# Kernel tuning notes

Hardware: AMD Instinct MI355X
Metric: run time of the kernel (lower is better)

The kernel has to match this reference:

```python
import jax, jax.numpy as jnp
import numpy as np

B, S, D = 1, 2048, 1024   # batch, seq, hidden_size
I = 2048                  # intermediate_size (mlp1 emits 2*I, SwiGLU halves)
E = 8                     # num_experts
K = 2                     # experts_per_token
LIMIT = 7.0               # swiglu_limit
ALPHA = 1.702             # gpt-oss swiglu alpha
EPS = 1e-5                # RMSNorm eps


def setup_inputs() -> dict:
    key = jax.random.key(0)
    ks = jax.random.split(key, 4)
    s = 0.02
    return {
        "x": jax.random.normal(ks[0], (B, S, D), jnp.float32),
        "norm_scale": jnp.ones((D,), jnp.float32),
        "gate_w": jax.random.normal(ks[1], (D, E), jnp.float32) * s,
        "gate_b": jnp.zeros((E,), jnp.float32),
        "mlp1_w": jax.random.normal(ks[2], (E, D, 2 * I), jnp.float32) * s,
        "mlp1_b": jnp.zeros((E, 2 * I), jnp.float32),
        "mlp2_w": jax.random.normal(ks[3], (E, I, D), jnp.float32) * s,
        "mlp2_b": jnp.zeros((E, D), jnp.float32),
    }


def _swiglu(h):
    # gpt-oss interleaved SwiGLU with clamp limit
    x_glu = jnp.minimum(h[..., ::2], LIMIT)
    x_lin = jnp.clip(h[..., 1::2], -LIMIT, LIMIT)
    return x_glu * jax.nn.sigmoid(ALPHA * x_glu) * (x_lin + 1.0)


def _moe(t, gate_w, gate_b, mlp1_w, mlp1_b, mlp2_w, mlp2_b):
    T = t.shape[0]
    logits = t @ gate_w + gate_b                 # [T, E]
    top_v, top_i = jax.lax.top_k(logits, K)      # [T, K]
    probs = jax.nn.softmax(top_v, axis=-1)       # softmax over selected experts
    # dense routing-weight matrix, zero for unselected experts
    w = jnp.zeros((T, E), t.dtype).at[jnp.arange(T)[:, None], top_i].set(probs)

    def body(acc, ew):
        w1, b1, w2, b2, we = ew                  # per-expert params + weights [T]
        h = _swiglu(t @ w1 + b1)                 # [T, I]
        y = h @ w2 + b2                          # [T, D]
        return acc + we[:, None] * y, None

    acc0 = jnp.zeros((T, t.shape[1]), t.dtype)
    acc, _ = jax.lax.scan(body, acc0, (mlp1_w, mlp1_b, mlp2_w, mlp2_b, w.T))
    return acc


def reference(x, norm_scale, gate_w, gate_b, mlp1_w, mlp1_b, mlp2_w, mlp2_b):
    Bx, Sx, Dx = x.shape
    ms = jnp.mean(x * x, axis=-1, keepdims=True)
    t = (x * jax.lax.rsqrt(ms + EPS) * norm_scale).reshape(Bx * Sx, Dx)
    y = _moe(t, gate_w, gate_b, mlp1_w, mlp1_b, mlp2_w, mlp2_b)
    return x + y.reshape(Bx, Sx, Dx)
```

## Files before the change

### kernel.cpp

```cpp
#include <hip/hip_runtime.h>
#include <hip/hip_bf16.h>

typedef unsigned short u16;
typedef __attribute__((ext_vector_type(4))) unsigned short u16x4;
typedef __attribute__((ext_vector_type(8))) unsigned short u16x8;
typedef __attribute__((ext_vector_type(8))) short bf16x8;
typedef __attribute__((ext_vector_type(4))) float f32x4;

#define DEV static __device__ __forceinline__

DEV float bf2f(u16 b){ union{unsigned u; float f;} c; c.u = ((unsigned)b) << 16; return c.f; }
DEV u16 f2bf(float f){ union{float f; unsigned u;} c; c.f = f; unsigned u = c.u; u += 0x7FFF + ((u >> 16) & 1); return (u16)(u >> 16); }
DEV u16 f2bfh(float f){ union { __hip_bfloat16 h; u16 u; } c; c.h = __float2bfloat16(f); return c.u; }
DEV float getc(float4 v, int c){ return c == 0 ? v.x : c == 1 ? v.y : c == 2 ? v.z : v.w; }

DEV void gload16(const void* g, void* l){
  __builtin_amdgcn_global_load_lds((const __attribute__((address_space(1))) unsigned int*)g,
                                   (__attribute__((address_space(3))) unsigned int*)l, 16, 0, 0);
}

__global__ __launch_bounds__(256) void k_rms(
    const float* __restrict__ x, const float* __restrict__ nsc,
    const float* __restrict__ gw, const float* __restrict__ gb,
    u16* __restrict__ t, int* __restrict__ topi, float* __restrict__ topp)
{
  const int token = blockIdx.x, tid = threadIdx.x;
  const int wv = tid >> 6, lane = tid & 63;
  const float4 xv = *(const float4*)&x[(size_t)token * 1024 + tid * 4];
  float f[4] = {xv.x, xv.y, xv.z, xv.w};
  float ss = f[0]*f[0] + f[1]*f[1] + f[2]*f[2] + f[3]*f[3];
  #pragma unroll
  for (int o = 32; o > 0; o >>= 1) ss += __shfl_down(ss, o, 64);
  __shared__ float red[4];
  __shared__ float s_rs;
  if (lane == 0) red[wv] = ss;
  __syncthreads();
  if (tid == 0) s_rs = rsqrtf((red[0] + red[1] + red[2] + red[3]) * (1.0f / 1024.0f) + 1e-5f);
  __syncthreads();
  const float rs = s_rs;
  const float4 sv = *(const float4*)&nsc[tid * 4];
  const float sc[4] = {sv.x, sv.y, sv.z, sv.w};
  float tf[4]; u16x4 tv;
  #pragma unroll
  for (int j = 0; j < 4; ++j){ tf[j] = f[j] * rs * sc[j]; tv[j] = f2bf(tf[j]); }
  *(u16x4*)&t[(size_t)token * 1024 + tid * 4] = tv;

  float la[8] = {0,0,0,0,0,0,0,0};
  #pragma unroll
  for (int j = 0; j < 4; ++j){
    const int k = tid * 4 + j;
    const float4 g0 = *(const float4*)&gw[k * 8];
    const float4 g1 = *(const float4*)&gw[k * 8 + 4];
    la[0] += tf[j] * g0.x; la[1] += tf[j] * g0.y; la[2] += tf[j] * g0.z; la[3] += tf[j] * g0.w;
    la[4] += tf[j] * g1.x; la[5] += tf[j] * g1.y; la[6] += tf[j] * g1.z; la[7] += tf[j] * g1.w;
  }
  #pragma unroll
  for (int o = 32; o > 0; o >>= 1)
    #pragma unroll
    for (int e = 0; e < 8; ++e) la[e] += __shfl_down(la[e], o, 64);
  __shared__ float lred[4][8];
  if (lane == 0){
    #pragma unroll
    for (int e = 0; e < 8; ++e) lred[wv][e] = la[e];
  }
  __syncthreads();
  if (tid == 0){
    float lg[8];
    #pragma unroll
    for (int e = 0; e < 8; ++e) lg[e] = lred[0][e] + lred[1][e] + lred[2][e] + lred[3][e] + gb[e];
    int i0 = 0;
    for (int e = 1; e < 8; ++e) if (lg[e] > lg[i0]) i0 = e;
    int i1 = -1;
    for (int e = 0; e < 8; ++e) if (e != i0 && (i1 < 0 || lg[e] > lg[i1])) i1 = e;
    const float d = __expf(lg[i1] - lg[i0]);
    const float p0 = 1.0f / (1.0f + d);
    topi[token * 2] = i0; topi[token * 2 + 1] = i1;
    topp[token * 2] = p0; topp[token * 2 + 1] = d * p0;
  }
}

__global__ __launch_bounds__(256) void k_route(
    const int* __restrict__ topi, const float* __restrict__ topp,
    int* __restrict__ cnt, int* __restrict__ offs, int* __restrict__ tok_of,
    float* __restrict__ wt_of, int* __restrict__ slot_of, int* __restrict__ posg)
{
  __shared__ int c[8];
  __shared__ int o[8];
  const int tid = threadIdx.x;
  if (tid < 8) c[tid] = 0;
  __syncthreads();
  for (int a = tid; a < 4096; a += 256){
    int e = topi[a];
    posg[a] = atomicAdd(&c[e], 1);
  }
  __syncthreads();
  if (tid == 0){
    int run = 0;
    for (int e = 0; e < 8; ++e){ o[e] = run; offs[e] = run; cnt[e] = c[e]; run += c[e]; }
  }
  __syncthreads();
  for (int a = tid; a < 4096; a += 256){
    int e = topi[a];
    int s = o[e] + posg[a];
    tok_of[s] = a >> 1;
    wt_of[s] = topp[a];
    slot_of[a] = s;
  }
}

__global__ __launch_bounds__(256) void k_gemm1(
    const u16* __restrict__ t, const float* __restrict__ w1, const float* __restrict__ b1,
    const int* __restrict__ cnt, const int* __restrict__ offs, const int* __restrict__ tok_of,
    u16* __restrict__ h)
{
  const int e = blockIdx.z;
  const int count = cnt[e];
  const int m0 = blockIdx.y * 128;
  if (m0 >= count) return;
  const int off = offs[e];
  const int n0 = blockIdx.x * 128;

  __shared__ __attribute__((aligned(16))) u16 As[128 * 64];
  __shared__ __attribute__((aligned(16))) u16 Bs[128 * 64];

  const int tid = threadIdx.x, wv = tid >> 6, lane = tid & 63;
  const int arl = lane >> 3;
  const int axu = (lane & 7) ^ arl;

  const u16* asrc[4];
  u16* adst[4];
  #pragma unroll
  for (int i = 0; i < 4; ++i){
    const int rr = i * 32 + wv * 8 + arl;
    int r = m0 + rr; if (r > count - 1) r = count - 1;
    asrc[i] = t + (size_t)tok_of[off + r] * 1024 + axu * 8;
    adst[i] = &As[(i * 32 + wv * 8) * 64];
  }

  const int tkq = tid >> 5;
  const int tnb = (tid & 31) * 4;
  const float* bsrc = w1 + (size_t)e * (1024 * 4096) + (size_t)(tkq * 8) * 4096 + n0 + tnb;

  const int wm = wv & 1, wn = wv >> 1;
  const int fr = lane & 15, q = lane >> 4;

  f32x4 acc[4][4];
  #pragma unroll
  for (int a = 0; a < 4; ++a)
    #pragma unroll
    for (int b = 0; b < 4; ++b) acc[a][b] = (f32x4){0.f, 0.f, 0.f, 0.f};

  for (int k0 = 0; k0 < 1024; k0 += 64){
    #pragma unroll
    for (int i = 0; i < 4; ++i){ gload16(asrc[i], adst[i]); asrc[i] += 64; }
    const float4 fv0 = *(const float4*)(bsrc);
    const float4 fv1 = *(const float4*)(bsrc + 4096);
    const float4 fv2 = *(const float4*)(bsrc + 2 * 4096);
    const float4 fv3 = *(const float4*)(bsrc + 3 * 4096);
    const float4 fv4 = *(const float4*)(bsrc + 4 * 4096);
    const float4 fv5 = *(const float4*)(bsrc + 5 * 4096);
    const float4 fv6 = *(const float4*)(bsrc + 6 * 4096);
    const float4 fv7 = *(const float4*)(bsrc + 7 * 4096);
    bsrc += (size_t)64 * 4096;
    #pragma unroll
    for (int c = 0; c < 4; ++c){
      const int nr = tnb + c;
      u16x8 wq;
      wq[0] = f2bfh(getc(fv0, c)); wq[1] = f2bfh(getc(fv1, c));
      wq[2] = f2bfh(getc(fv2, c)); wq[3] = f2bfh(getc(fv3, c));
      wq[4] = f2bfh(getc(fv4, c)); wq[5] = f2bfh(getc(fv5, c));
      wq[6] = f2bfh(getc(fv6, c)); wq[7] = f2bfh(getc(fv7, c));
      *(u16x8*)((char*)Bs + nr * 128 + ((tkq ^ ((nr >> 1) & 7)) << 4)) = wq;
    }
    __syncthreads();
    #pragma unroll
    for (int hh = 0; hh < 2; ++hh){
      const int puA = (((hh * 4) + q) ^ (fr & 7)) * 8;
      const int puB = (((hh * 4) + q) ^ ((fr >> 1) & 7)) * 8;
      bf16x8 af[4], bq[4];
      #pragma unroll
      for (int fm = 0; fm < 4; ++fm) af[fm] = *(const bf16x8*)&As[(wm * 64 + fm * 16 + fr) * 64 + puA];
      #pragma unroll
      for (int fn = 0; fn < 4; ++fn) bq[fn] = *(const bf16x8*)&Bs[(wn * 64 + fn * 16 + fr) * 64 + puB];
      #pragma unroll
      for (int fm = 0; fm < 4; ++fm)
        #pragma unroll
        for (int fn = 0; fn < 4; ++fn)
          acc[fm][fn] = __builtin_amdgcn_mfma_f32_16x16x32_bf16(af[fm], bq[fn], acc[fm][fn], 0, 0, 0);
    }
    __syncthreads();
  }

  const int cb = n0 + wn * 64 + fr;
  float b1v[4];
  #pragma unroll
  for (int fn = 0; fn < 4; ++fn) b1v[fn] = b1[e * 4096 + cb + fn * 16];
  const int rq = q * 4;
  const bool ev = ((lane & 1) == 0);
  #pragma unroll
  for (int fm = 0; fm < 4; ++fm)
    #pragma unroll
    for (int fn = 0; fn < 4; ++fn)
      #pragma unroll
      for (int r = 0; r < 4; ++r){
        const float val = acc[fm][fn][r] + b1v[fn];
        const float oth = __shfl_xor(val, 1, 64);
        if (ev){
          const int row = m0 + wm * 64 + fm * 16 + rq + r;
          if (row < count){
            const float g = fminf(val, 7.0f);
            const float l = fminf(fmaxf(oth, -7.0f), 7.0f);
            const float o = g / (1.0f + __expf(-1.702f * g)) * (l + 1.0f);
            h[(size_t)(off + row) * 2048 + ((cb + fn * 16) >> 1)] = f2bf(o);
          }
        }
      }
}

__global__ __launch_bounds__(256) void k_gemm2(
    const u16* __restrict__ h, const float* __restrict__ w2, const float* __restrict__ b2,
    const int* __restrict__ cnt, const int* __restrict__ offs, const float* __restrict__ wt_of,
    u16* __restrict__ ys)
{
  const int e = blockIdx.z;
  const int count = cnt[e];
  const int m0 = blockIdx.y * 128;
  if (m0 >= count) return;
  const int off = offs[e];
  const int n0 = blockIdx.x * 64;

  __shared__ __attribute__((aligned(16))) u16 As[128 * 64];
  __shared__ __attribute__((aligned(16))) u16 Bs[64 * 64];

  const int tid = threadIdx.x, wv = tid >> 6, lane = tid & 63;
  const int arl = lane >> 3;
  const int axu = (lane & 7) ^ arl;

  const u16* asrc[4];
  u16* adst[4];
  #pragma unroll
  for (int i = 0; i < 4; ++i){
    const int rr = i * 32 + wv * 8 + arl;
    int r = m0 + rr; if (r > count - 1) r = count - 1;
    asrc[i] = h + (size_t)(off + r) * 2048 + axu * 8;
    adst[i] = &As[(i * 32 + wv * 8) * 64];
  }

  const int tkq = tid >> 4;
  const int tnb = (tid & 15) * 4;
  const float* bsrc = w2 + (size_t)e * (2048 * 1024) + (size_t)(tkq * 4) * 1024 + n0 + tnb;

  const int wm = wv & 1, wn = wv >> 1;
  const int fr = lane & 15, q = lane >> 4;

  f32x4 acc[4][2];
  #pragma unroll
  for (int a = 0; a < 4; ++a)
    #pragma unroll
    for (int b = 0; b < 2; ++b) acc[a][b] = (f32x4){0.f, 0.f, 0.f, 0.f};

  for (int k0 = 0; k0 < 2048; k0 += 64){
    #pragma unroll
    for (int i = 0; i < 4; ++i){ gload16(asrc[i], adst[i]); asrc[i] += 64; }
    const float4 g0 = *(const float4*)(bsrc);
    const float4 g1 = *(const float4*)(bsrc + 1024);
    const float4 g2 = *(const float4*)(bsrc + 2 * 1024);
    const float4 g3 = *(const float4*)(bsrc + 3 * 1024);
    bsrc += (size_t)64 * 1024;
    #pragma unroll
    for (int c = 0; c < 4; ++c){
      const int nr = tnb + c;
      u16x4 wd;
      wd[0] = f2bfh(getc(g0, c)); wd[1] = f2bfh(getc(g1, c));
      wd[2] = f2bfh(getc(g2, c)); wd[3] = f2bfh(getc(g3, c));
      *(u16x4*)((char*)Bs + nr * 128 + (((tkq >> 1) ^ ((nr >> 1) & 7)) << 4) + ((tkq & 1) << 3)) = wd;
    }
    __syncthreads();
    #pragma unroll
    for (int hh = 0; hh < 2; ++hh){
      const int puA = (((hh * 4) + q) ^ (fr & 7)) * 8;
      const int puB = (((hh * 4) + q) ^ ((fr >> 1) & 7)) * 8;
      bf16x8 af[4], bq[2];
      #pragma unroll
      for (int fm = 0; fm < 4; ++fm) af[fm] = *(const bf16x8*)&As[(wm * 64 + fm * 16 + fr) * 64 + puA];
      #pragma unroll
      for (int fn = 0; fn < 2; ++fn) bq[fn] = *(const bf16x8*)&Bs[(wn * 32 + fn * 16 + fr) * 64 + puB];
      #pragma unroll
      for (int fm = 0; fm < 4; ++fm)
        #pragma unroll
        for (int fn = 0; fn < 2; ++fn)
          acc[fm][fn] = __builtin_amdgcn_mfma_f32_16x16x32_bf16(af[fm], bq[fn], acc[fm][fn], 0, 0, 0);
    }
    __syncthreads();
  }

  const int cb = n0 + wn * 32 + fr;
  float b2v[2];
  #pragma unroll
  for (int fn = 0; fn < 2; ++fn) b2v[fn] = b2[e * 1024 + cb + fn * 16];
  const int rq = q * 4;
  #pragma unroll
  for (int fm = 0; fm < 4; ++fm)
    #pragma unroll
    for (int rr = 0; rr < 4; ++rr){
      const int row = m0 + wm * 64 + fm * 16 + rq + rr;
      if (row < count){
        const float wt = wt_of[off + row];
        #pragma unroll
        for (int fn = 0; fn < 2; ++fn){
          const float v = (acc[fm][fn][rr] + b2v[fn]) * wt;
          ys[(size_t)(off + row) * 1024 + cb + fn * 16] = f2bf(v);
        }
      }
    }
}

__global__ __launch_bounds__(256) void k_final(
    const float* __restrict__ x, const u16* __restrict__ ys,
    const int* __restrict__ slot_of, float* __restrict__ out)
{
  const int gid = blockIdx.x * 256 + threadIdx.x;
  const int token = gid >> 8;
  const int c0 = (gid & 255) * 4;
  const int s0 = slot_of[token * 2], s1 = slot_of[token * 2 + 1];
  const float4 xv = *(const float4*)&x[(size_t)token * 1024 + c0];
  const u16x4 y0 = *(const u16x4*)&ys[(size_t)s0 * 1024 + c0];
  const u16x4 y1 = *(const u16x4*)&ys[(size_t)s1 * 1024 + c0];
  float4 o;
  o.x = xv.x + bf2f(y0[0]) + bf2f(y1[0]);
  o.y = xv.y + bf2f(y0[1]) + bf2f(y1[1]);
  o.z = xv.z + bf2f(y0[2]) + bf2f(y1[2]);
  o.w = xv.w + bf2f(y0[3]) + bf2f(y1[3]);
  *(float4*)&out[(size_t)token * 1024 + c0] = o;
}

extern "C" void kernel_launch(void* const* d_in, const int* in_sizes, int n_in,
                              void* d_out, int out_size, void* d_ws, size_t ws_size,
                              hipStream_t stream)
{
  const float* x   = (const float*)d_in[0];
  const float* nsc = (const float*)d_in[1];
  const float* gw  = (const float*)d_in[2];
  const float* gb  = (const float*)d_in[3];
  const float* w1  = (const float*)d_in[4];
  const float* b1  = (const float*)d_in[5];
  const float* w2  = (const float*)d_in[6];
  const float* b2  = (const float*)d_in[7];
  float* out = (float*)d_out;
  char* ws = (char*)d_ws;

  size_t o = 0;
  auto alloc = [&](size_t bytes){ size_t r = o; o = (o + bytes + 255) & ~(size_t)255; return r; };
  const size_t o_t    = alloc((size_t)2048 * 1024 * 2);
  const size_t o_h    = alloc((size_t)4096 * 2048 * 2);
  const size_t o_ys   = alloc((size_t)4096 * 1024 * 2);
  const size_t o_topi = alloc(4096 * 4);
  const size_t o_topp = alloc(4096 * 4);
  const size_t o_posg = alloc(4096 * 4);
  const size_t o_tok  = alloc(4096 * 4);
  const size_t o_wt   = alloc(4096 * 4);
  const size_t o_slot = alloc(4096 * 4);
  const size_t o_cnt  = alloc(8 * 4);
  const size_t o_offs = alloc(8 * 4);
  if (ws_size < o) return;

  u16*   t_ws  = (u16*)(ws + o_t);
  u16*   h_ws  = (u16*)(ws + o_h);
  u16*   ys    = (u16*)(ws + o_ys);
  int*   topi  = (int*)(ws + o_topi);
  float* topp  = (float*)(ws + o_topp);
  int*   posg  = (int*)(ws + o_posg);
  int*   tok   = (int*)(ws + o_tok);
  float* wt    = (float*)(ws + o_wt);
  int*   slot  = (int*)(ws + o_slot);
  int*   cnt   = (int*)(ws + o_cnt);
  int*   offs  = (int*)(ws + o_offs);

  k_rms  <<<2048, 256, 0, stream>>>(x, nsc, gw, gb, t_ws, topi, topp);
  k_route<<<1, 256, 0, stream>>>(topi, topp, cnt, offs, tok, wt, slot, posg);
  k_gemm1<<<dim3(32, 16, 8), 256, 0, stream>>>(t_ws, w1, b1, cnt, offs, tok, h_ws);
  k_gemm2<<<dim3(16, 16, 8), 256, 0, stream>>>(h_ws, w2, b2, cnt, offs, wt, ys);
  k_final<<<2048, 256, 0, stream>>>(x, ys, slot, out);
}
```

Baseline: 384.2 us.

## Double-buffer LDS tiles in expert GEMM kernels to overlap loads with MFMA

Both expert GEMM kernels now use two LDS buffers for the A and B tiles. The next K-slice's global-to-LDS A loads and the fp32 weight register loads are issued before the MFMA compute on the current buffer, and the converted B tile is written afterwards. This drops one barrier per iteration and hides global memory latency behind compute. In exchange it doubles LDS use (64KB in gemm1), which may lower occupancy, and it raises register pressure from the held weight registers.

```diff
diff --git a/kernel.cpp b/kernel.cpp
--- a/kernel.cpp
+++ b/kernel.cpp
@@ -120,21 +120,22 @@
   const int off = offs[e];
   const int n0 = blockIdx.x * 128;
 
-  __shared__ __attribute__((aligned(16))) u16 As[128 * 64];
-  __shared__ __attribute__((aligned(16))) u16 Bs[128 * 64];
+  __shared__ __attribute__((aligned(16))) u16 As[2][128 * 64];
+  __shared__ __attribute__((aligned(16))) u16 Bs[2][128 * 64];
 
   const int tid = threadIdx.x, wv = tid >> 6, lane = tid & 63;
   const int arl = lane >> 3;
   const int axu = (lane & 7) ^ arl;
 
   const u16* asrc[4];
-  u16* adst[4];
+  u16* adst[2][4];
   #pragma unroll
   for (int i = 0; i < 4; ++i){
     const int rr = i * 32 + wv * 8 + arl;
     int r = m0 + rr; if (r > count - 1) r = count - 1;
     asrc[i] = t + (size_t)tok_of[off + r] * 1024 + axu * 8;
-    adst[i] = &As[(i * 32 + wv * 8) * 64];
+    adst[0][i] = &As[0][(i * 32 + wv * 8) * 64];
+    adst[1][i] = &As[1][(i * 32 + wv * 8) * 64];
   }
 
   const int tkq = tid >> 5;
@@ -150,46 +151,63 @@
     #pragma unroll
     for (int b = 0; b < 4; ++b) acc[a][b] = (f32x4){0.f, 0.f, 0.f, 0.f};
 
-  for (int k0 = 0; k0 < 1024; k0 += 64){
-    #pragma unroll
-    for (int i = 0; i < 4; ++i){ gload16(asrc[i], adst[i]); asrc[i] += 64; }
-    const float4 fv0 = *(const float4*)(bsrc);
-    const float4 fv1 = *(const float4*)(bsrc + 4096);
-    const float4 fv2 = *(const float4*)(bsrc + 2 * 4096);
-    const float4 fv3 = *(const float4*)(bsrc + 3 * 4096);
-    const float4 fv4 = *(const float4*)(bsrc + 4 * 4096);
-    const float4 fv5 = *(const float4*)(bsrc + 5 * 4096);
-    const float4 fv6 = *(const float4*)(bsrc + 6 * 4096);
-    const float4 fv7 = *(const float4*)(bsrc + 7 * 4096);
+  auto loadB = [&](float4* fv){
+    #pragma unroll
+    for (int j = 0; j < 8; ++j) fv[j] = *(const float4*)(bsrc + (size_t)j * 4096);
     bsrc += (size_t)64 * 4096;
+  };
+  auto writeB = [&](u16* B, const float4* fv){
     #pragma unroll
     for (int c = 0; c < 4; ++c){
       const int nr = tnb + c;
       u16x8 wq;
-      wq[0] = f2bfh(getc(fv0, c)); wq[1] = f2bfh(getc(fv1, c));
-      wq[2] = f2bfh(getc(fv2, c)); wq[3] = f2bfh(getc(fv3, c));
-      wq[4] = f2bfh(getc(fv4, c)); wq[5] = f2bfh(getc(fv5, c));
-      wq[6] = f2bfh(getc(fv6, c)); wq[7] = f2bfh(getc(fv7, c));
-      *(u16x8*)((char*)Bs + nr * 128 + ((tkq ^ ((nr >> 1) & 7)) << 4)) = wq;
+      wq[0] = f2bfh(getc(fv[0], c)); wq[1] = f2bfh(getc(fv[1], c));
+      wq[2] = f2bfh(getc(fv[2], c)); wq[3] = f2bfh(getc(fv[3], c));
+      wq[4] = f2bfh(getc(fv[4], c)); wq[5] = f2bfh(getc(fv[5], c));
+      wq[6] = f2bfh(getc(fv[6], c)); wq[7] = f2bfh(getc(fv[7], c));
+      *(u16x8*)((char*)B + nr * 128 + ((tkq ^ ((nr >> 1) & 7)) << 4)) = wq;
     }
-    __syncthreads();
+  };
+  auto compute = [&](const u16* A, const u16* B){
     #pragma unroll
     for (int hh = 0; hh < 2; ++hh){
       const int puA = (((hh * 4) + q) ^ (fr & 7)) * 8;
       const int puB = (((hh * 4) + q) ^ ((fr >> 1) & 7)) * 8;
       bf16x8 af[4], bq[4];
       #pragma unroll
-      for (int fm = 0; fm < 4; ++fm) af[fm] = *(const bf16x8*)&As[(wm * 64 + fm * 16 + fr) * 64 + puA];
-      #pragma unroll
-      for (int fn = 0; fn < 4; ++fn) bq[fn] = *(const bf16x8*)&Bs[(wn * 64 + fn * 16 + fr) * 64 + puB];
+      for (int fm = 0; fm < 4; ++fm) af[fm] = *(const bf16x8*)&A[(wm * 64 + fm * 16 + fr) * 64 + puA];
+      #pragma unroll
+      for (int fn = 0; fn < 4; ++fn) bq[fn] = *(const bf16x8*)&B[(wn * 64 + fn * 16 + fr) * 64 + puB];
       #pragma unroll
       for (int fm = 0; fm < 4; ++fm)
         #pragma unroll
         for (int fn = 0; fn < 4; ++fn)
           acc[fm][fn] = __builtin_amdgcn_mfma_f32_16x16x32_bf16(af[fm], bq[fn], acc[fm][fn], 0, 0, 0);
     }
+  };
+
+  {
+    #pragma unroll
+    for (int i = 0; i < 4; ++i){ gload16(asrc[i], adst[0][i]); asrc[i] += 64; }
+    float4 fv[8];
+    loadB(fv);
+    writeB(Bs[0], fv);
+  }
+  __syncthreads();
+
+  int cur = 0;
+  for (int tt = 0; tt < 15; ++tt){
+    const int nxt = cur ^ 1;
+    #pragma unroll
+    for (int i = 0; i < 4; ++i){ gload16(asrc[i], adst[nxt][i]); asrc[i] += 64; }
+    float4 fv[8];
+    loadB(fv);
+    compute(As[cur], Bs[cur]);
+    writeB(Bs[nxt], fv);
     __syncthreads();
-  }
+    cur = nxt;
+  }
+  compute(As[cur], Bs[cur]);
 
   const int cb = n0 + wn * 64 + fr;
   float b1v[4];
@@ -229,21 +247,22 @@
   const int off = offs[e];
   const int n0 = blockIdx.x * 64;
 
-  __shared__ __attribute__((aligned(16))) u16 As[128 * 64];
-  __shared__ __attribute__((aligned(16))) u16 Bs[64 * 64];
+  __shared__ __attribute__((aligned(16))) u16 As[2][128 * 64];
+  __shared__ __attribute__((aligned(16))) u16 Bs[2][64 * 64];
 
   const int tid = threadIdx.x, wv = tid >> 6, lane = tid & 63;
   const int arl = lane >> 3;
   const int axu = (lane & 7) ^ arl;
 
   const u16* asrc[4];
-  u16* adst[4];
+  u16* adst[2][4];
   #pragma unroll
   for (int i = 0; i < 4; ++i){
     const int rr = i * 32 + wv * 8 + arl;
     int r = m0 + rr; if (r > count - 1) r = count - 1;
     asrc[i] = h + (size_t)(off + r) * 2048 + axu * 8;
-    adst[i] = &As[(i * 32 + wv * 8) * 64];
+    adst[0][i] = &As[0][(i * 32 + wv * 8) * 64];
+    adst[1][i] = &As[1][(i * 32 + wv * 8) * 64];
   }
 
   const int tkq = tid >> 4;
@@ -259,40 +278,61 @@
     #pragma unroll
     for (int b = 0; b < 2; ++b) acc[a][b] = (f32x4){0.f, 0.f, 0.f, 0.f};
 
-  for (int k0 = 0; k0 < 2048; k0 += 64){
-    #pragma unroll
-    for (int i = 0; i < 4; ++i){ gload16(asrc[i], adst[i]); asrc[i] += 64; }
-    const float4 g0 = *(const float4*)(bsrc);
-    const float4 g1 = *(const float4*)(bsrc + 1024);
-    const float4 g2 = *(const float4*)(bsrc + 2 * 1024);
-    const float4 g3 = *(const float4*)(bsrc + 3 * 1024);
+  auto loadB = [&](float4* fv){
+    #pragma unroll
+    for (int j = 0; j < 4; ++j) fv[j] = *(const float4*)(bsrc + (size_t)j * 1024);
     bsrc += (size_t)64 * 1024;
+  };
+  auto writeB = [&](u16* B, const float4* fv){
     #pragma unroll
     for (int c = 0; c < 4; ++c){
       const int nr = tnb + c;
       u16x4 wd;
-      wd[0] = f2bfh(getc(g0, c)); wd[1] = f2bfh(getc(g1, c));
-      wd[2] = f2bfh(getc(g2, c)); wd[3] = f2bfh(getc(g3, c));
-      *(u16x4*)((char*)Bs + nr * 128 + (((tkq >> 1) ^ ((nr >> 1) & 7)) << 4) + ((tkq & 1) << 3)) = wd;
+      wd[0] = f2bfh(getc(fv[0], c)); wd[1] = f2bfh(getc(fv[1], c));
+      wd[2] = f2bfh(getc(fv[2], c)); wd[3] = f2bfh(getc(fv[3], c));
+      *(u16x4*)((char*)B + nr * 128 + (((tkq >> 1) ^ ((nr >> 1) & 7)) << 4) + ((tkq & 1) << 3)) = wd;
     }
-    __syncthreads();
+  };
+  auto compute = [&](const u16* A, const u16* B){
     #pragma unroll
     for (int hh = 0; hh < 2; ++hh){
       const int puA = (((hh * 4) + q) ^ (fr & 7)) * 8;
       const int puB = (((hh * 4) + q) ^ ((fr >> 1) & 7)) * 8;
       bf16x8 af[4], bq[2];
       #pragma unroll
-      for (int fm = 0; fm < 4; ++fm) af[fm] = *(const bf16x8*)&As[(wm * 64 + fm * 16 + fr) * 64 + puA];
-      #pragma unroll
-      for (int fn = 0; fn < 2; ++fn) bq[fn] = *(const bf16x8*)&Bs[(wn * 32 + fn * 16 + fr) * 64 + puB];
+      for (int fm = 0; fm < 4; ++fm) af[fm] = *(const bf16x8*)&A[(wm * 64 + fm * 16 + fr) * 64 + puA];
+      #pragma unroll
+      for (int fn = 0; fn < 2; ++fn) bq[fn] = *(const bf16x8*)&B[(wn * 32 + fn * 16 + fr) * 64 + puB];
       #pragma unroll
       for (int fm = 0; fm < 4; ++fm)
         #pragma unroll
         for (int fn = 0; fn < 2; ++fn)
           acc[fm][fn] = __builtin_amdgcn_mfma_f32_16x16x32_bf16(af[fm], bq[fn], acc[fm][fn], 0, 0, 0);
     }
+  };
+
+  {
+    #pragma unroll
+    for (int i = 0; i < 4; ++i){ gload16(asrc[i], adst[0][i]); asrc[i] += 64; }
+    float4 fv[4];
+    loadB(fv);
+    writeB(Bs[0], fv);
+  }
+  __syncthreads();
+
+  int cur = 0;
+  for (int tt = 0; tt < 31; ++tt){
+    const int nxt = cur ^ 1;
+    #pragma unroll
+    for (int i = 0; i < 4; ++i){ gload16(asrc[i], adst[nxt][i]); asrc[i] += 64; }
+    float4 fv[4];
+    loadB(fv);
+    compute(As[cur], Bs[cur]);
+    writeB(Bs[nxt], fv);
     __syncthreads();
-  }
+    cur = nxt;
+  }
+  compute(As[cur], Bs[cur]);
 
   const int cb = n0 + wn * 32 + fr;
   float b2v[2];
```

After: 371.3 us. 3.3% less time.

## Double-buffer gemm2 LDS tiles and remap block order to spread experts

Applied to the files above, without the earlier changes.

In gemm2, the A and B LDS tiles are double-buffered. The next k-slice's global loads are issued before computing the current slice, which overlaps memory latency with MFMA work and drops one barrier per iteration. Both GEMM kernels also remap the flat block id so that consecutive blocks interleave across experts, aiming to balance work and cache behaviour across CUs. The cost is twice the LDS in gemm2, which may lower occupancy. The remap also assumes fixed grid dimensions (32/16 column blocks, 16 row blocks, 8 experts).

```diff
diff --git a/kernel.cpp b/kernel.cpp
--- a/kernel.cpp
+++ b/kernel.cpp
@@ -113,12 +113,14 @@
     const int* __restrict__ cnt, const int* __restrict__ offs, const int* __restrict__ tok_of,
     u16* __restrict__ h)
 {
-  const int e = blockIdx.z;
+  const int fid = blockIdx.x + (blockIdx.y << 5) + (blockIdx.z << 9);
+  const int L = ((fid & 7) << 9) + (fid >> 3);
+  const int e = L >> 9;
+  const int n0 = ((L >> 4) & 31) * 128;
+  const int m0 = (L & 15) * 128;
   const int count = cnt[e];
-  const int m0 = blockIdx.y * 128;
   if (m0 >= count) return;
   const int off = offs[e];
-  const int n0 = blockIdx.x * 128;
 
   __shared__ __attribute__((aligned(16))) u16 As[128 * 64];
   __shared__ __attribute__((aligned(16))) u16 Bs[128 * 64];
@@ -222,28 +224,31 @@
     const int* __restrict__ cnt, const int* __restrict__ offs, const float* __restrict__ wt_of,
     u16* __restrict__ ys)
 {
-  const int e = blockIdx.z;
+  const int fid = blockIdx.x + (blockIdx.y << 4) + (blockIdx.z << 8);
+  const int L = ((fid & 7) << 8) + (fid >> 3);
+  const int e = L >> 8;
+  const int n0 = ((L >> 4) & 15) * 64;
+  const int m0 = (L & 15) * 128;
   const int count = cnt[e];
-  const int m0 = blockIdx.y * 128;
   if (m0 >= count) return;
   const int off = offs[e];
-  const int n0 = blockIdx.x * 64;
-
-  __shared__ __attribute__((aligned(16))) u16 As[128 * 64];
-  __shared__ __attribute__((aligned(16))) u16 Bs[64 * 64];
+
+  __shared__ __attribute__((aligned(16))) u16 As[2][128 * 64];
+  __shared__ __attribute__((aligned(16))) u16 Bs[2][64 * 64];
 
   const int tid = threadIdx.x, wv = tid >> 6, lane = tid & 63;
   const int arl = lane >> 3;
   const int axu = (lane & 7) ^ arl;
 
   const u16* asrc[4];
-  u16* adst[4];
+  u16* adst[2][4];
   #pragma unroll
   for (int i = 0; i < 4; ++i){
     const int rr = i * 32 + wv * 8 + arl;
     int r = m0 + rr; if (r > count - 1) r = count - 1;
     asrc[i] = h + (size_t)(off + r) * 2048 + axu * 8;
-    adst[i] = &As[(i * 32 + wv * 8) * 64];
+    adst[0][i] = &As[0][(i * 32 + wv * 8) * 64];
+    adst[1][i] = &As[1][(i * 32 + wv * 8) * 64];
   }
 
   const int tkq = tid >> 4;
@@ -259,40 +264,61 @@
     #pragma unroll
     for (int b = 0; b < 2; ++b) acc[a][b] = (f32x4){0.f, 0.f, 0.f, 0.f};
 
-  for (int k0 = 0; k0 < 2048; k0 += 64){
-    #pragma unroll
-    for (int i = 0; i < 4; ++i){ gload16(asrc[i], adst[i]); asrc[i] += 64; }
-    const float4 g0 = *(const float4*)(bsrc);
-    const float4 g1 = *(const float4*)(bsrc + 1024);
-    const float4 g2 = *(const float4*)(bsrc + 2 * 1024);
-    const float4 g3 = *(const float4*)(bsrc + 3 * 1024);
+  auto loadB = [&](float4* fv){
+    #pragma unroll
+    for (int j = 0; j < 4; ++j) fv[j] = *(const float4*)(bsrc + (size_t)j * 1024);
     bsrc += (size_t)64 * 1024;
+  };
+  auto writeB = [&](u16* B, const float4* fv){
     #pragma unroll
     for (int c = 0; c < 4; ++c){
       const int nr = tnb + c;
       u16x4 wd;
-      wd[0] = f2bfh(getc(g0, c)); wd[1] = f2bfh(getc(g1, c));
-      wd[2] = f2bfh(getc(g2, c)); wd[3] = f2bfh(getc(g3, c));
-      *(u16x4*)((char*)Bs + nr * 128 + (((tkq >> 1) ^ ((nr >> 1) & 7)) << 4) + ((tkq & 1) << 3)) = wd;
+      wd[0] = f2bfh(getc(fv[0], c)); wd[1] = f2bfh(getc(fv[1], c));
+      wd[2] = f2bfh(getc(fv[2], c)); wd[3] = f2bfh(getc(fv[3], c));
+      *(u16x4*)((char*)B + nr * 128 + (((tkq >> 1) ^ ((nr >> 1) & 7)) << 4) + ((tkq & 1) << 3)) = wd;
     }
-    __syncthreads();
+  };
+  auto compute = [&](const u16* A, const u16* B){
     #pragma unroll
     for (int hh = 0; hh < 2; ++hh){
       const int puA = (((hh * 4) + q) ^ (fr & 7)) * 8;
       const int puB = (((hh * 4) + q) ^ ((fr >> 1) & 7)) * 8;
       bf16x8 af[4], bq[2];
       #pragma unroll
-      for (int fm = 0; fm < 4; ++fm) af[fm] = *(const bf16x8*)&As[(wm * 64 + fm * 16 + fr) * 64 + puA];
-      #pragma unroll
-      for (int fn = 0; fn < 2; ++fn) bq[fn] = *(const bf16x8*)&Bs[(wn * 32 + fn * 16 + fr) * 64 + puB];
+      for (int fm = 0; fm < 4; ++fm) af[fm] = *(const bf16x8*)&A[(wm * 64 + fm * 16 + fr) * 64 + puA];
+      #pragma unroll
+      for (int fn = 0; fn < 2; ++fn) bq[fn] = *(const bf16x8*)&B[(wn * 32 + fn * 16 + fr) * 64 + puB];
       #pragma unroll
       for (int fm = 0; fm < 4; ++fm)
         #pragma unroll
         for (int fn = 0; fn < 2; ++fn)
           acc[fm][fn] = __builtin_amdgcn_mfma_f32_16x16x32_bf16(af[fm], bq[fn], acc[fm][fn], 0, 0, 0);
     }
+  };
+
+  {
+    #pragma unroll
+    for (int i = 0; i < 4; ++i){ gload16(asrc[i], adst[0][i]); asrc[i] += 64; }
+    float4 fv[4];
+    loadB(fv);
+    writeB(Bs[0], fv);
+  }
+  __syncthreads();
+
+  int cur = 0;
+  for (int tt = 0; tt < 31; ++tt){
+    const int nxt = cur ^ 1;
+    #pragma unroll
+    for (int i = 0; i < 4; ++i){ gload16(asrc[i], adst[nxt][i]); asrc[i] += 64; }
+    float4 fv[4];
+    loadB(fv);
+    compute(As[cur], Bs[cur]);
+    writeB(Bs[nxt], fv);
     __syncthreads();
-  }
+    cur = nxt;
+  }
+  compute(As[cur], Bs[cur]);
 
   const int cb = n0 + wn * 32 + fr;
   float b2v[2];
```

Result: slower. 430.8 us (+12.1%).
